# Kernel tuning notes

Hardware: AMD Instinct MI355X
Metric: run time of the kernel (lower is better)

The kernel has to match this reference:

```python
import jax, jax.numpy as jnp
import numpy as np

COMP_TOKEN_ID = 7
R = 8
LORA_ALPHA = 16
SCALING = LORA_ALPHA / R  # 2.0


def setup_inputs() -> dict:
    key = jax.random.key(0)
    k1, k2, k3, k4, k5, k6 = jax.random.split(key, 6)
    B, S, D_IN, D_OUT = 4, 4096, 4096, 4096
    x = jax.random.normal(k1, (B, S, D_IN), dtype=jnp.float32)
    ids = jax.random.randint(k2, (B, S), 0, 64, dtype=jnp.int64)
    W = jax.random.normal(k3, (D_OUT, D_IN), dtype=jnp.float32) * (1.0 / np.sqrt(D_IN))
    b = jax.random.normal(k4, (D_OUT,), dtype=jnp.float32) * 0.02
    lora_A = jax.random.normal(k5, (R, D_IN), dtype=jnp.float32) * (1.0 / np.sqrt(D_IN))
    lora_B = jax.random.normal(k6, (D_OUT, R), dtype=jnp.float32) * 0.02
    return {"x": x, "ids": ids, "W": W, "b": b, "lora_A": lora_A, "lora_B": lora_B}


def reference(x, ids, W, b, lora_A, lora_B):
    # Base frozen linear: [B,S,d_in] @ [d_in,d_out] -> [B,S,d_out]
    base = jnp.einsum('bsi,oi->bso', x, W) + b
    # LoRA path (dropout is identity in eval mode): x @ A.T @ B.T * scaling
    lora = jnp.einsum('bsr,or->bso', jnp.einsum('bsi,ri->bsr', x, lora_A), lora_B) * SCALING
    # Per-token gate: only compression tokens get the LoRA update
    mask = (ids == COMP_TOKEN_ID).astype(x.dtype)[..., None]  # [B,S,1]
    return base + lora * mask
```

## Files before the change

kernel.cpp:

```cpp
#include <hip/hip_runtime.h>
#include <hip/hip_bf16.h>
#include <stdint.h>


typedef __attribute__((ext_vector_type(8))) __bf16 bf16x8;
typedef __attribute__((ext_vector_type(4))) float f32x4;

#define M_DIM 16384
#define K_DIM 4096
#define N_DIM 4096
#define BM 256
#define BN 256
#define BK 64
#define NT2 (K_DIM / BK)

__global__ __launch_bounds__(256) void cvt_wa(
    const float* __restrict__ W, __hip_bfloat16* __restrict__ Wb,
    const float* __restrict__ A, __hip_bfloat16* __restrict__ Ab) {
    int b = blockIdx.x;
    if (b < 1024) {
        int i = b * 256 + threadIdx.x;
        const int n8 = N_DIM * K_DIM / 8;
        const int stride = 1024 * 256;
        for (; i < n8; i += stride) {
            const float4* p = (const float4*)(W + (size_t)i * 8);
            float4 v0 = p[0], v1 = p[1];
            bf16x8 o;
            o[0] = (__bf16)v0.x; o[1] = (__bf16)v0.y; o[2] = (__bf16)v0.z; o[3] = (__bf16)v0.w;
            o[4] = (__bf16)v1.x; o[5] = (__bf16)v1.y; o[6] = (__bf16)v1.z; o[7] = (__bf16)v1.w;
            *(bf16x8*)((__hip_bfloat16*)Wb + (size_t)i * 8) = o;
        }
    } else {
        int i = (b - 1024) * 256 + threadIdx.x;
        if (i < 8 * K_DIM / 8) {
            const float4* p = (const float4*)(A + (size_t)i * 8);
            float4 v0 = p[0], v1 = p[1];
            bf16x8 o;
            o[0] = (__bf16)v0.x; o[1] = (__bf16)v0.y; o[2] = (__bf16)v0.z; o[3] = (__bf16)v0.w;
            o[4] = (__bf16)v1.x; o[5] = (__bf16)v1.y; o[6] = (__bf16)v1.z; o[7] = (__bf16)v1.w;
            *(bf16x8*)((__hip_bfloat16*)Ab + (size_t)i * 8) = o;
        }
    }
}

__global__ __launch_bounds__(256) void cvt_x_xa(
    const float* __restrict__ x, const int* __restrict__ ids,
    const __hip_bfloat16* __restrict__ Abf,
    __hip_bfloat16* __restrict__ Xb, float* __restrict__ xa) {
    __shared__ __hip_bfloat16 As[8 * 4096];
    int tid = threadIdx.x;
    for (int i = tid; i < 8 * 4096 / 8; i += 256)
        *(bf16x8*)(As + i * 8) = *(const bf16x8*)(Abf + i * 8);
    __syncthreads();

    int wave = tid >> 6, lane = tid & 63;
#pragma unroll
    for (int rr = 0; rr < 2; rr++) {
        int row = blockIdx.x * 8 + wave * 2 + rr;
        const float* xr = x + (size_t)row * K_DIM;
        __hip_bfloat16* xo = Xb + (size_t)row * K_DIM;
        float s[8] = {0.f, 0.f, 0.f, 0.f, 0.f, 0.f, 0.f, 0.f};
#pragma unroll
        for (int j = 0; j < 8; j++) {
            int k = j * 512 + lane * 8;
            float4 v0 = *(const float4*)(xr + k);
            float4 v1 = *(const float4*)(xr + k + 4);
            bf16x8 o;
            o[0] = (__bf16)v0.x; o[1] = (__bf16)v0.y; o[2] = (__bf16)v0.z; o[3] = (__bf16)v0.w;
            o[4] = (__bf16)v1.x; o[5] = (__bf16)v1.y; o[6] = (__bf16)v1.z; o[7] = (__bf16)v1.w;
            *(bf16x8*)(xo + k) = o;
#pragma unroll
            for (int r = 0; r < 8; r++) {
                bf16x8 av = *(const bf16x8*)(As + r * 4096 + k);
                s[r] += v0.x * (float)av[0] + v0.y * (float)av[1] + v0.z * (float)av[2] + v0.w * (float)av[3]
                      + v1.x * (float)av[4] + v1.y * (float)av[5] + v1.z * (float)av[6] + v1.w * (float)av[7];
            }
        }
#pragma unroll
        for (int r = 0; r < 8; r++) {
            float v = s[r];
            for (int off = 32; off; off >>= 1) v += __shfl_down(v, off);
            s[r] = v;
        }
        if (lane == 0) {
            float gate = (ids[row] == 7) ? 2.0f : 0.0f;
#pragma unroll
            for (int r = 0; r < 8; r++) xa[(size_t)row * 8 + r] = s[r] * gate;
        }
    }
}

__device__ __forceinline__ void gload_lds16(const void* g, void* l) {
    __builtin_amdgcn_global_load_lds(
        (const __attribute__((address_space(1))) unsigned int*)g,
        (__attribute__((address_space(3))) unsigned int*)l, 16, 0, 0);
}

#define LGKMW(n) asm volatile("s_waitcnt lgkmcnt(" #n ")" ::: "memory")
#define VMCW(n)  asm volatile("s_waitcnt vmcnt(" #n ")" ::: "memory")
#define SB0()    __builtin_amdgcn_sched_barrier(0)
#define BAR()    __builtin_amdgcn_s_barrier()
#define PRIO(p)  __builtin_amdgcn_s_setprio(p)

__global__ __launch_bounds__(512, 1) void gemm_bias_lora(
    const __hip_bfloat16* __restrict__ Xb,
    const __hip_bfloat16* __restrict__ Wb,
    const float* __restrict__ bias,
    const float* __restrict__ xa,
    const float* __restrict__ loraB,
    float* __restrict__ out) {
    __shared__ char smem[147456];

    int tid = threadIdx.x;
    int bid = blockIdx.x;
    int swz = (bid & 7) * 128 + (bid >> 3);
    int n_tile = swz & 15;
    int m_tile = swz >> 4;
    int m_base = m_tile * BM, n_base = n_tile * BN;
    int wave = tid >> 6, lane = tid & 63;
    int wr = wave >> 2, wc = wave & 3;
    int l15 = lane & 15, lhi = lane >> 4;
    int l8 = lane >> 3;
    int cx = ((lane & 7) ^ l8) * 16;
    int pswz0 = ((lhi)     ^ (l15 & 7)) * 16;
    int pswz1 = ((4 + lhi) ^ (l15 & 7)) * 16;
    int psA = wr ? pswz1 : pswz0;
    int psB = wr ? pswz0 : pswz1;

    f32x4 acc[8][4] = {};

    const char* Abase = (const char*)(Xb + (size_t)m_base * K_DIM);
    const char* Bbase = (const char*)(Wb + (size_t)n_base * K_DIM);

    auto stage_Au = [&](int kt, int mq, char* ubase) {
#pragma unroll
        for (int j = 0; j < 2; j++) {
            int rg = wave * 2 + j;
            int rl = rg * 8 + l8;
            int g = (rl < 64) ? (mq * 64 + rl) : (128 + mq * 64 + (rl - 64));
            gload_lds16(Abase + (size_t)g * (K_DIM * 2) + (size_t)kt * 128 + cx,
                        ubase + rg * 1024 + lane * 16);
        }
    };
    auto stage_B = [&](int kt, int h, int buf) {
        char* ub = smem + 81920 + buf * 32768 + h * 16384;
#pragma unroll
        for (int j = 0; j < 2; j++) {
            int rg = wave * 2 + j;
            int row = h * 128 + rg * 8 + l8;
            gload_lds16(Bbase + (size_t)row * (K_DIM * 2) + (size_t)kt * 128 + cx,
                        ub + rg * 1024 + lane * 16);
        }
    };

    stage_Au(0, 0, smem);
    stage_B(0, 0, 0); stage_B(0, 1, 0);
    stage_Au(0, 1, smem + 49152);
    stage_Au(1, 0, smem + 16384);
    VMCW(2);
    BAR();

    bf16x8 af0[4], af1[4], bf0[4], bf1[4];
    int s0 = 0;

    for (int t = 0; t < NT2; t++) {
        int cb = t & 1, nb = cb ^ 1;
        int s2 = s0 + 2; if (s2 >= 3) s2 -= 3;
        const char* aU0 = smem + s0 * 16384 + (wr * 64 + l15) * 128;
        const char* aU1 = smem + 49152 + cb * 16384 + (wr * 64 + l15) * 128;
        const char* bRb = smem + 81920 + cb * 32768 + (wc * 64 + l15) * 128;

#pragma unroll
        for (int mi = 0; mi < 4; mi++) af0[mi] = *(const bf16x8*)(aU0 + mi * 2048 + psA);
#pragma unroll
        for (int ni = 0; ni < 4; ni++) bf0[ni] = *(const bf16x8*)(bRb + ni * 2048 + psA);
#pragma unroll
        for (int mi = 0; mi < 4; mi++) af1[mi] = *(const bf16x8*)(aU1 + mi * 2048 + psA);
        if (t + 1 < NT2) stage_B(t + 1, 0, nb);
        LGKMW(4); SB0();
        PRIO(1);
#pragma unroll
        for (int mi = 0; mi < 4; mi++)
#pragma unroll
            for (int ni = 0; ni < 4; ni++)
                acc[mi][ni] = __builtin_amdgcn_mfma_f32_16x16x32_bf16(af0[mi], bf0[ni], acc[mi][ni], 0, 0, 0);
        PRIO(0);

#pragma unroll
        for (int mi = 0; mi < 4; mi++) af0[mi] = *(const bf16x8*)(aU0 + mi * 2048 + psB);
#pragma unroll
        for (int ni = 0; ni < 4; ni++) bf1[ni] = *(const bf16x8*)(bRb + ni * 2048 + psB);
        if (t + 1 < NT2) { stage_B(t + 1, 1, nb); stage_Au(t + 1, 1, smem + 49152 + nb * 16384); }
        LGKMW(8); SB0();
        PRIO(1);
#pragma unroll
        for (int mi = 0; mi < 4; mi++)
#pragma unroll
            for (int ni = 0; ni < 4; ni++)
                acc[4 + mi][ni] = __builtin_amdgcn_mfma_f32_16x16x32_bf16(af1[mi], bf0[ni], acc[4 + mi][ni], 0, 0, 0);
        PRIO(0);

#pragma unroll
        for (int mi = 0; mi < 4; mi++) af1[mi] = *(const bf16x8*)(aU1 + mi * 2048 + psB);
        LGKMW(4); SB0();
        PRIO(1);
#pragma unroll
        for (int mi = 0; mi < 4; mi++)
#pragma unroll
            for (int ni = 0; ni < 4; ni++)
                acc[mi][ni] = __builtin_amdgcn_mfma_f32_16x16x32_bf16(af0[mi], bf1[ni], acc[mi][ni], 0, 0, 0);
        PRIO(0);

        if (t + 2 < NT2) stage_Au(t + 2, 0, smem + s2 * 16384);
        LGKMW(0); SB0();
        PRIO(1);
#pragma unroll
        for (int mi = 0; mi < 4; mi++)
#pragma unroll
            for (int ni = 0; ni < 4; ni++)
                acc[4 + mi][ni] = __builtin_amdgcn_mfma_f32_16x16x32_bf16(af1[mi], bf1[ni], acc[4 + mi][ni], 0, 0, 0);
        PRIO(0);
        if (t < NT2 - 2) { VMCW(2); } else { VMCW(0); }
        BAR();

        s0 = s0 + 1; if (s0 >= 3) s0 -= 3;
    }

    int wrow = m_base + wr * 128;
    int wcol = n_base + wc * 64;
    float bv[4];
    float4 lb0[4], lb1[4];
#pragma unroll
    for (int ni = 0; ni < 4; ni++) {
        int n = wcol + ni * 16 + l15;
        bv[ni] = bias[n];
        lb0[ni] = *(const float4*)(loraB + (size_t)n * 8);
        lb1[ni] = *(const float4*)(loraB + (size_t)n * 8 + 4);
    }
#pragma unroll
    for (int mi = 0; mi < 8; mi++) {
#pragma unroll
        for (int r = 0; r < 4; r++) {
            int m = wrow + mi * 16 + lhi * 4 + r;
            float4 xa0 = *(const float4*)(xa + (size_t)m * 8);
            float4 xa1 = *(const float4*)(xa + (size_t)m * 8 + 4);
#pragma unroll
            for (int ni = 0; ni < 4; ni++) {
                int n = wcol + ni * 16 + l15;
                float lora = xa0.x * lb0[ni].x + xa0.y * lb0[ni].y + xa0.z * lb0[ni].z + xa0.w * lb0[ni].w
                           + xa1.x * lb1[ni].x + xa1.y * lb1[ni].y + xa1.z * lb1[ni].z + xa1.w * lb1[ni].w;
                out[(size_t)m * N_DIM + n] = acc[mi][ni][r] + bv[ni] + lora;
            }
        }
    }
}

__global__ void fallback_kernel(const float* __restrict__ x, const int* __restrict__ ids,
                                const float* __restrict__ W, const float* __restrict__ b,
                                const float* __restrict__ A, const float* __restrict__ B8,
                                float* __restrict__ out) {
    __shared__ float xs[K_DIM];
    __shared__ float xa_s[8];
    int row = blockIdx.y;
    int t = threadIdx.x;
    const float* xr = x + (size_t)row * K_DIM;
    for (int k = t; k < K_DIM; k += 256) xs[k] = xr[k];
    __syncthreads();
    if (t < 8) {
        float s = 0.f;
        for (int k = 0; k < K_DIM; k++) s += xs[k] * A[t * K_DIM + k];
        xa_s[t] = (ids[row] == 7) ? s * 2.0f : 0.0f;
    }
    __syncthreads();
    int col = blockIdx.x * 256 + t;
    const float* wr = W + (size_t)col * K_DIM;
    float acc = 0.f;
    for (int k = 0; k < K_DIM; k++) acc += xs[k] * wr[k];
    float lora = 0.f;
#pragma unroll
    for (int rr = 0; rr < 8; rr++) lora += xa_s[rr] * B8[col * 8 + rr];
    out[(size_t)row * N_DIM + col] = acc + b[col] + lora;
}

extern "C" void kernel_launch(void* const* d_in, const int* in_sizes, int n_in,
                              void* d_out, int out_size, void* d_ws, size_t ws_size,
                              hipStream_t stream) {
    const float* x   = (const float*)d_in[0];
    const int*   ids = (const int*)d_in[1];
    const float* W   = (const float*)d_in[2];
    const float* b   = (const float*)d_in[3];
    const float* lA  = (const float*)d_in[4];
    const float* lB  = (const float*)d_in[5];
    float* out = (float*)d_out;

    size_t wb_bytes = (size_t)N_DIM * K_DIM * 2;
    size_t xb_bytes = (size_t)M_DIM * K_DIM * 2;
    size_t xa_bytes = (size_t)M_DIM * 8 * 4;
    size_t ab_bytes = (size_t)8 * K_DIM * 2;

    if (ws_size >= wb_bytes + xb_bytes + xa_bytes + ab_bytes) {
        __hip_bfloat16* Wb  = (__hip_bfloat16*)d_ws;
        __hip_bfloat16* Xb  = (__hip_bfloat16*)((char*)d_ws + wb_bytes);
        float*          xav = (float*)((char*)d_ws + wb_bytes + xb_bytes);
        __hip_bfloat16* Abf = (__hip_bfloat16*)((char*)d_ws + wb_bytes + xb_bytes + xa_bytes);

        cvt_wa<<<1024 + 16, 256, 0, stream>>>(W, Wb, lA, Abf);
        cvt_x_xa<<<M_DIM / 8, 256, 0, stream>>>(x, ids, Abf, Xb, xav);
        gemm_bias_lora<<<(M_DIM / BM) * (N_DIM / BN), 512, 0, stream>>>(Xb, Wb, b, xav, lB, out);
    } else {
        fallback_kernel<<<dim3(N_DIM / 256, M_DIM), 256, 0, stream>>>(x, ids, W, b, lA, lB, out);
    }
}
```

Baseline: 572.3 us.

## Shrink GEMM tile to 128x256 with BK=32 and simpler three-stage pipeline

Replaces the 256x256x64 tile, its split A/B staging and four-phase interleaved MFMA loop with a 128x256x32 tile. Each k-step now does one load and compute phase over a uniform three-slot LDS ring, with a new swizzle and block remap for twice as many tiles. The LDS footprint is halved and launch bounds ask for four blocks per CU, aiming at higher occupancy to hide latency. The costs are lower operand reuse per tile, twice as many barriers per K, and a possible tight register cap that could cause spills.

```diff
diff --git a/kernel.cpp b/kernel.cpp
--- a/kernel.cpp
+++ b/kernel.cpp
@@ -9,10 +9,10 @@
 #define M_DIM 16384
 #define K_DIM 4096
 #define N_DIM 4096
-#define BM 256
+#define BM 128
 #define BN 256
-#define BK 64
-#define NT2 (K_DIM / BK)
+#define BK 32
+#define NT3 (K_DIM / BK)
 
 __global__ __launch_bounds__(256) void cvt_wa(
     const float* __restrict__ W, __hip_bfloat16* __restrict__ Wb,
@@ -102,131 +102,80 @@
 #define BAR()    __builtin_amdgcn_s_barrier()
 #define PRIO(p)  __builtin_amdgcn_s_setprio(p)
 
-__global__ __launch_bounds__(512, 1) void gemm_bias_lora(
+__global__ __launch_bounds__(512, 4) void gemm_bias_lora(
     const __hip_bfloat16* __restrict__ Xb,
     const __hip_bfloat16* __restrict__ Wb,
     const float* __restrict__ bias,
     const float* __restrict__ xa,
     const float* __restrict__ loraB,
     float* __restrict__ out) {
-    __shared__ char smem[147456];
+    __shared__ char smem[73728];
 
     int tid = threadIdx.x;
     int bid = blockIdx.x;
-    int swz = (bid & 7) * 128 + (bid >> 3);
+    int swz = (bid & 7) * 256 + (bid >> 3);
     int n_tile = swz & 15;
     int m_tile = swz >> 4;
     int m_base = m_tile * BM, n_base = n_tile * BN;
     int wave = tid >> 6, lane = tid & 63;
     int wr = wave >> 2, wc = wave & 3;
     int l15 = lane & 15, lhi = lane >> 4;
-    int l8 = lane >> 3;
-    int cx = ((lane & 7) ^ l8) * 16;
-    int pswz0 = ((lhi)     ^ (l15 & 7)) * 16;
-    int pswz1 = ((4 + lhi) ^ (l15 & 7)) * 16;
-    int psA = wr ? pswz1 : pswz0;
-    int psB = wr ? pswz0 : pswz1;
-
-    f32x4 acc[8][4] = {};
+    int cxs = ((lane & 3) ^ ((lane >> 3) & 3)) * 16;
+    int pos = (lhi ^ ((l15 >> 1) & 3)) << 4;
+    int lrow = lane >> 2;
+
+    f32x4 acc[4][4] = {};
 
     const char* Abase = (const char*)(Xb + (size_t)m_base * K_DIM);
     const char* Bbase = (const char*)(Wb + (size_t)n_base * K_DIM);
 
-    auto stage_Au = [&](int kt, int mq, char* ubase) {
+    auto stage = [&](int kt, int slot) {
+        char* sb = smem + slot * 24576;
+        size_t kb = (size_t)kt * 64 + cxs;
+        {
+            int rl = wave * 16 + lrow;
+            gload_lds16(Abase + (size_t)rl * 8192 + kb, sb + wave * 1024 + lane * 16);
+        }
 #pragma unroll
         for (int j = 0; j < 2; j++) {
             int rg = wave * 2 + j;
-            int rl = rg * 8 + l8;
-            int g = (rl < 64) ? (mq * 64 + rl) : (128 + mq * 64 + (rl - 64));
-            gload_lds16(Abase + (size_t)g * (K_DIM * 2) + (size_t)kt * 128 + cx,
-                        ubase + rg * 1024 + lane * 16);
+            int rl = rg * 16 + lrow;
+            gload_lds16(Bbase + (size_t)rl * 8192 + kb, sb + 8192 + rg * 1024 + lane * 16);
         }
     };
-    auto stage_B = [&](int kt, int h, int buf) {
-        char* ub = smem + 81920 + buf * 32768 + h * 16384;
-#pragma unroll
-        for (int j = 0; j < 2; j++) {
-            int rg = wave * 2 + j;
-            int row = h * 128 + rg * 8 + l8;
-            gload_lds16(Bbase + (size_t)row * (K_DIM * 2) + (size_t)kt * 128 + cx,
-                        ub + rg * 1024 + lane * 16);
-        }
-    };
-
-    stage_Au(0, 0, smem);
-    stage_B(0, 0, 0); stage_B(0, 1, 0);
-    stage_Au(0, 1, smem + 49152);
-    stage_Au(1, 0, smem + 16384);
-    VMCW(2);
+
+    stage(0, 0);
+    stage(1, 1);
+    VMCW(3);
     BAR();
 
-    bf16x8 af0[4], af1[4], bf0[4], bf1[4];
     int s0 = 0;
-
-    for (int t = 0; t < NT2; t++) {
-        int cb = t & 1, nb = cb ^ 1;
+    for (int t = 0; t < NT3; t++) {
         int s2 = s0 + 2; if (s2 >= 3) s2 -= 3;
-        const char* aU0 = smem + s0 * 16384 + (wr * 64 + l15) * 128;
-        const char* aU1 = smem + 49152 + cb * 16384 + (wr * 64 + l15) * 128;
-        const char* bRb = smem + 81920 + cb * 32768 + (wc * 64 + l15) * 128;
-
-#pragma unroll
-        for (int mi = 0; mi < 4; mi++) af0[mi] = *(const bf16x8*)(aU0 + mi * 2048 + psA);
-#pragma unroll
-        for (int ni = 0; ni < 4; ni++) bf0[ni] = *(const bf16x8*)(bRb + ni * 2048 + psA);
-#pragma unroll
-        for (int mi = 0; mi < 4; mi++) af1[mi] = *(const bf16x8*)(aU1 + mi * 2048 + psA);
-        if (t + 1 < NT2) stage_B(t + 1, 0, nb);
-        LGKMW(4); SB0();
-        PRIO(1);
-#pragma unroll
-        for (int mi = 0; mi < 4; mi++)
-#pragma unroll
-            for (int ni = 0; ni < 4; ni++)
-                acc[mi][ni] = __builtin_amdgcn_mfma_f32_16x16x32_bf16(af0[mi], bf0[ni], acc[mi][ni], 0, 0, 0);
-        PRIO(0);
-
-#pragma unroll
-        for (int mi = 0; mi < 4; mi++) af0[mi] = *(const bf16x8*)(aU0 + mi * 2048 + psB);
-#pragma unroll
-        for (int ni = 0; ni < 4; ni++) bf1[ni] = *(const bf16x8*)(bRb + ni * 2048 + psB);
-        if (t + 1 < NT2) { stage_B(t + 1, 1, nb); stage_Au(t + 1, 1, smem + 49152 + nb * 16384); }
-        LGKMW(8); SB0();
-        PRIO(1);
-#pragma unroll
-        for (int mi = 0; mi < 4; mi++)
-#pragma unroll
-            for (int ni = 0; ni < 4; ni++)
-                acc[4 + mi][ni] = __builtin_amdgcn_mfma_f32_16x16x32_bf16(af1[mi], bf0[ni], acc[4 + mi][ni], 0, 0, 0);
-        PRIO(0);
-
-#pragma unroll
-        for (int mi = 0; mi < 4; mi++) af1[mi] = *(const bf16x8*)(aU1 + mi * 2048 + psB);
-        LGKMW(4); SB0();
-        PRIO(1);
-#pragma unroll
-        for (int mi = 0; mi < 4; mi++)
-#pragma unroll
-            for (int ni = 0; ni < 4; ni++)
-                acc[mi][ni] = __builtin_amdgcn_mfma_f32_16x16x32_bf16(af0[mi], bf1[ni], acc[mi][ni], 0, 0, 0);
-        PRIO(0);
-
-        if (t + 2 < NT2) stage_Au(t + 2, 0, smem + s2 * 16384);
+        const char* aR = smem + s0 * 24576 + (wr * 64 + l15) * 64;
+        const char* bR = smem + s0 * 24576 + 8192 + (wc * 64 + l15) * 64;
+
+        bf16x8 af[4], bf[4];
+#pragma unroll
+        for (int mi = 0; mi < 4; mi++) af[mi] = *(const bf16x8*)(aR + mi * 1024 + pos);
+#pragma unroll
+        for (int ni = 0; ni < 4; ni++) bf[ni] = *(const bf16x8*)(bR + ni * 1024 + pos);
+        if (t + 2 < NT3) stage(t + 2, s2);
         LGKMW(0); SB0();
         PRIO(1);
 #pragma unroll
         for (int mi = 0; mi < 4; mi++)
 #pragma unroll
             for (int ni = 0; ni < 4; ni++)
-                acc[4 + mi][ni] = __builtin_amdgcn_mfma_f32_16x16x32_bf16(af1[mi], bf1[ni], acc[4 + mi][ni], 0, 0, 0);
+                acc[mi][ni] = __builtin_amdgcn_mfma_f32_16x16x32_bf16(af[mi], bf[ni], acc[mi][ni], 0, 0, 0);
         PRIO(0);
-        if (t < NT2 - 2) { VMCW(2); } else { VMCW(0); }
+        if (t < NT3 - 2) { VMCW(3); } else { VMCW(0); }
         BAR();
 
         s0 = s0 + 1; if (s0 >= 3) s0 -= 3;
     }
 
-    int wrow = m_base + wr * 128;
+    int wrow = m_base + wr * 64;
     int wcol = n_base + wc * 64;
     float bv[4];
     float4 lb0[4], lb1[4];
@@ -238,7 +187,7 @@
         lb1[ni] = *(const float4*)(loraB + (size_t)n * 8 + 4);
     }
 #pragma unroll
-    for (int mi = 0; mi < 8; mi++) {
+    for (int mi = 0; mi < 4; mi++) {
 #pragma unroll
         for (int r = 0; r < 4; r++) {
             int m = wrow + mi * 16 + lhi * 4 + r;
```

New measurement: 705.7 us. +23.3%, slower.
